# Kernel optimization log

Measured on AMD Instinct MI355X. Metric: run time of the kernel, lower is better.

## Reference

```python
import math
import jax, jax.numpy as jnp
import numpy as np

B, L, D, H = 2, 2048, 1024, 16
DK = D // H
N_TYPES = 6  # token types; < 3 => prompt (U/O/E), >= 3 => item (I)


def setup_inputs() -> dict:
    key = jax.random.key(0)
    ks = jax.random.split(key, 8)
    w_scale = 0.02
    return {
        "x": jax.random.normal(ks[0], (B, L, D), dtype=jnp.float32),
        "token_types": jax.random.randint(ks[1], (B, L), 0, N_TYPES, dtype=jnp.int32),
        "seq_lens": jax.random.randint(ks[2], (B,), L // 2, L + 1, dtype=jnp.int32),
        "W_q": jax.random.normal(ks[3], (D, D), dtype=jnp.float32) * w_scale,
        "W_k": jax.random.normal(ks[4], (D, D), dtype=jnp.float32) * w_scale,
        "W_v": jax.random.normal(ks[5], (D, D), dtype=jnp.float32) * w_scale,
        "W_u": jax.random.normal(ks[6], (D, D), dtype=jnp.float32) * w_scale,
        "W_o": jax.random.normal(ks[7], (D, D), dtype=jnp.float32) * w_scale,
    }


def reference(x, token_types, seq_lens, W_q, W_k, W_v, W_u, W_o):
    b, l, d = x.shape
    neg = jnp.finfo(x.dtype).min

    def proj(W):  # torch Linear (no bias): y = x @ W.T -> (b, H, l, dk)
        return jnp.einsum("bld,ed->ble", x, W).reshape(b, l, H, DK).transpose(0, 2, 1, 3)

    Q, K, V, U = proj(W_q), proj(W_k), proj(W_v), proj(W_u)

    scores = jnp.einsum("bhid,bhjd->bhij", Q, K) / math.sqrt(DK)  # (b,H,l,l)

    # Hybrid mask: causal (-inf above diagonal), but 0 wherever key j is a
    # prompt token (prompt<->prompt bidirectional, item->prompt allowed).
    is_prompt = token_types < 3                      # (b, l)
    causal = jnp.where(jnp.triu(jnp.ones((l, l), dtype=bool), k=1), neg, 0.0).astype(x.dtype)
    mask = jnp.where(is_prompt[:, None, :], jnp.asarray(0.0, x.dtype), causal[None, :, :])  # (b,l,l)
    scores = scores + mask[:, None, :, :]

    # Padding mask on key positions j >= seq_len
    pad = jnp.arange(l)[None, :] >= seq_lens[:, None]  # (b, l)
    scores = jnp.where(pad[:, None, None, :], neg, scores)

    attn = jax.nn.softmax(scores, axis=-1)
    out = jnp.einsum("bhij,bhjd->bhid", attn, V) * U   # HSTU pointwise gating
    out = out.transpose(0, 2, 1, 3).reshape(b, l, d)
    return jnp.einsum("bld,ed->ble", out, W_o)
```

## Files before the change

kernel.cpp:

```cpp
#include <hip/hip_runtime.h>


#define L_SEQ 2048

typedef __attribute__((ext_vector_type(8))) short bf16x8;
typedef __attribute__((ext_vector_type(8))) unsigned short u16x8;
typedef __attribute__((ext_vector_type(4))) float f32x4;
typedef __attribute__((ext_vector_type(16))) float f32x16;

#if __has_builtin(__builtin_amdgcn_exp2f)
#define EXP2F __builtin_amdgcn_exp2f
#else
#define EXP2F __builtin_exp2f
#endif

__device__ __forceinline__ unsigned short f2bf(float f) {
  union { float f; unsigned u; } c; c.f = f;
  unsigned r = c.u + 0x7FFFu + ((c.u >> 16) & 1u);
  return (unsigned short)(r >> 16);
}
__device__ __forceinline__ float bf2f(unsigned short h) {
  union { unsigned u; float f; } c; c.u = ((unsigned)h) << 16;
  return c.f;
}

__device__ __forceinline__ void async16(const void* g, void* l) {
  __builtin_amdgcn_global_load_lds((__attribute__((address_space(1))) void*)g,
                                   (__attribute__((address_space(3))) void*)l,
                                   16, 0, 0);
}

__device__ __forceinline__ unsigned cvtpk_bf16(float lo, float hi) {
  unsigned r; asm("v_cvt_pk_bf16_f32 %0, %1, %2" : "=v"(r) : "v"(lo), "v"(hi));
  return r;
}

__global__ __launch_bounds__(256) void cvt_all(
    const float* __restrict__ x,
    const float* __restrict__ wq, const float* __restrict__ wk,
    const float* __restrict__ wv, const float* __restrict__ wu,
    const float* __restrict__ wo,
    unsigned short* __restrict__ xb, unsigned short* __restrict__ wcat,
    const int* __restrict__ tt, const int* __restrict__ sl,
    unsigned* __restrict__ allowed) {
  if (blockIdx.x >= 9216) {
    const int k = blockIdx.x - 9216;
    const int wv64 = (k << 2) + (threadIdx.x >> 6);
    const int b = wv64 >> 5, w32 = wv64 & 31;
    const int lane = threadIdx.x & 63;
    const int j = w32 * 64 + lane;
    const unsigned long long m = __ballot((tt[b * L_SEQ + j] < 3) && (j < sl[b]));
    if (lane == 0) {
      allowed[b * 64 + 2 * w32]     = (unsigned)m;
      allowed[b * 64 + 2 * w32 + 1] = (unsigned)(m >> 32);
    }
    return;
  }
  const int seg = blockIdx.x >> 10;
  const float* s;
  unsigned short* d;
  float sc = 1.0f;
  if (seg < 4)      { s = x + (size_t)seg * 1048576;  d = xb + (size_t)seg * 1048576; }
  else {
    const int ws = seg - 4;
    s = ws == 0 ? wq : ws == 1 ? wk : ws == 2 ? wv : ws == 3 ? wu : wo;
    d = wcat + (size_t)ws * 1048576;
    if (ws == 0) sc = 0.18033688011112042f;
  }
  const int i = ((blockIdx.x & 1023) * 256 + threadIdx.x) * 4;
  const float4 v = *reinterpret_cast<const float4*>(s + i);
  ushort4 o;
  o.x = f2bf(v.x * sc); o.y = f2bf(v.y * sc); o.z = f2bf(v.z * sc); o.w = f2bf(v.w * sc);
  *reinterpret_cast<ushort4*>(d + i) = o;
}

__global__ __launch_bounds__(512, 2) void gemm256_bt(
    const unsigned short* __restrict__ A,
    const unsigned short* __restrict__ BT,
    unsigned short* __restrict__ Cb, int K)
{
  __shared__ char smem[131072];

  const int tid = threadIdx.x, w = tid >> 6, lane = tid & 63;
  const int lo = lane & 15, hi = lane >> 4;
  const int wm = w >> 2, wn = w & 3;
  const int d = blockIdx.x;
  const int lin = (d & 7) * 32 + (d >> 3);
  const int i0 = (lin >> 4) * 256, j0 = (lin & 15) * 256;

  const int rr = lane >> 3, ch = lane & 7;
  const int ksw = 8 * (ch ^ rr);

  auto stage = [&](int buf, int t) {
    const size_t k0 = (size_t)t * 64 + ksw;
    #pragma unroll
    for (int q = 0; q < 2; ++q) {
      const int p = 2 * w + q;
      const int row = 8 * p + rr;
      #pragma unroll
      for (int h = 0; h < 2; ++h) {
        async16(A  + (size_t)(i0 + h * 128 + row) * K + k0,
                smem + buf * 32768 + h * 16384 + p * 1024);
        async16(BT + (size_t)(j0 + h * 128 + row) * K + k0,
                smem + 65536 + buf * 32768 + h * 16384 + p * 1024);
      }
    }
  };

  f32x4 acc[8][4] = {};
  stage(0, 0);

  const int nt = K >> 6;
  for (int u = 0; u < nt; ++u) {
    const int buf = u & 1;
    if (u + 1 < nt) {
      stage(buf ^ 1, u + 1);
      asm volatile("s_waitcnt vmcnt(8)" ::: "memory");
    } else {
      asm volatile("s_waitcnt vmcnt(0)" ::: "memory");
    }
    __builtin_amdgcn_s_barrier();
    __builtin_amdgcn_sched_barrier(0);

    const char* Ah = smem + buf * 32768 + wm * 16384;
    const char* Bh = smem + 65536 + buf * 32768 + (wn >> 1) * 16384;
    const int brow0 = (wn & 1) * 64;

    bf16x8 bfr[4][2];
    #pragma unroll
    for (int n = 0; n < 4; ++n)
      #pragma unroll
      for (int ks = 0; ks < 2; ++ks)
        bfr[n][ks] = *reinterpret_cast<const bf16x8*>(
            Bh + (brow0 + n * 16 + lo) * 128 + 16 * ((ks * 4 + hi) ^ (lo & 7)));

    #pragma unroll
    for (int ph = 0; ph < 4; ++ph) {
      bf16x8 afr[2][2];
      #pragma unroll
      for (int mm = 0; mm < 2; ++mm)
        #pragma unroll
        for (int ks = 0; ks < 2; ++ks)
          afr[mm][ks] = *reinterpret_cast<const bf16x8*>(
              Ah + ((ph * 2 + mm) * 16 + lo) * 128 + 16 * ((ks * 4 + hi) ^ (lo & 7)));
      __builtin_amdgcn_s_barrier();
      __builtin_amdgcn_sched_barrier(0);
      __builtin_amdgcn_s_setprio(1);
      #pragma unroll
      for (int ks = 0; ks < 2; ++ks)
        #pragma unroll
        for (int mm = 0; mm < 2; ++mm)
          #pragma unroll
          for (int n = 0; n < 4; ++n)
            acc[ph * 2 + mm][n] = __builtin_amdgcn_mfma_f32_16x16x32_bf16(
                afr[mm][ks], bfr[n][ks], acc[ph * 2 + mm][n], 0, 0, 0);
      __builtin_amdgcn_s_setprio(0);
      __builtin_amdgcn_s_barrier();
      __builtin_amdgcn_sched_barrier(0);
    }
  }

  const int mi = (lin & 15) >> 2;
  const int cb0 = j0 & 1023;
  if (mi != 2) {
    unsigned short* base = Cb + (size_t)mi * 4194304;
    #pragma unroll
    for (int m = 0; m < 8; ++m) {
      const int row = i0 + wm * 128 + m * 16 + hi * 4;
      #pragma unroll
      for (int n = 0; n < 4; ++n) {
        const int col = cb0 + wn * 64 + n * 16 + lo;
        #pragma unroll
        for (int r = 0; r < 4; ++r)
          base[(size_t)(row + r) * 1024 + col] = f2bf(acc[m][n][r]);
      }
    }
  } else {
    #pragma unroll
    for (int m = 0; m < 8; ++m) {
      const int tl = (wm << 1) + (m >> 2);
      #pragma unroll
      for (int n = 0; n < 4; ++n) {
        const int dd = n * 16 + lo;
        char* ib = smem + (tl * 4 + wn) * 8192 + dd * 128;
        const int swd = dd & 7;
        #pragma unroll
        for (int r = 0; r < 4; ++r) {
          const int k = (m * 16 + hi * 4 + r) & 63;
          *(unsigned short*)(ib + 16 * ((k >> 3) ^ swd) + 2 * (k & 7)) =
              f2bf(acc[m][n][r]);
        }
      }
    }
    __builtin_amdgcn_s_barrier();
    unsigned short* V = Cb + (size_t)2 * 4194304;
    const int bI = i0 >> 11;
    const int t0 = (i0 & 2047) >> 6;
    const int h0 = cb0 >> 6;
    #pragma unroll
    for (int img = 0; img < 16; ++img) {
      const int tl = img >> 2, hl = img & 3;
      const size_t ob = ((size_t)(bI * 16 + h0 + hl) * 32 + (t0 + tl)) * 4096;
      *reinterpret_cast<u16x8*>(V + ob + tid * 8) =
          *reinterpret_cast<const u16x8*>(smem + img * 8192 + tid * 16);
    }
  }
}

template<int OUT_BF16, int MF>
__global__ __launch_bounds__(256) void gemm_bt(
    const unsigned short* __restrict__ A,
    const unsigned short* __restrict__ BT,
    float* __restrict__ Cf, unsigned short* __restrict__ Cb,
    int M, int N, int K, int cpx, int nbxm, int nbxs)
{
  __shared__ unsigned short As[2][MF * 32 * 32];
  __shared__ unsigned short Bs[2][128 * 32];

  const int tid = threadIdx.x;
  const int w = tid >> 6, lane = tid & 63;
  const int lo = lane & 15, hi = lane >> 4;
  const int d = blockIdx.x + gridDim.x * blockIdx.y;
  const int lin = (d & 7) * cpx + (d >> 3);
  const int i0 = (lin >> nbxs) * (MF * 32), j0 = (lin & nbxm) * 128;
  const int wr = w >> 1, wc = w & 1;
  const int rsub = lane >> 2, csub = (lane & 3) * 8;

  f32x4 acc[MF][4] = {};

  auto stage = [&](int buf, int k0) {
    #pragma unroll
    for (int q = 0; q < 2; ++q) {
      const int cB = w * 2 + q;
      async16(BT + (size_t)(j0 + cB * 16 + rsub) * K + k0 + csub, &Bs[buf][cB * 512]);
      if (q < MF / 2) {
        const int cA = w * (MF / 2) + q;
        async16(A + (size_t)(i0 + cA * 16 + rsub) * K + k0 + csub, &As[buf][cA * 512]);
      }
    }
  };

  stage(0, 0);
  __syncthreads();

  const int nt = K >> 5;
  for (int t = 0; t < nt; ++t) {
    const int buf = t & 1;
    if (t + 1 < nt) stage(buf ^ 1, (t + 1) << 5);
    bf16x8 a[MF], b[4];
    #pragma unroll
    for (int m = 0; m < MF; ++m)
      a[m] = *reinterpret_cast<const bf16x8*>(
          &As[buf][(wr * (MF * 16) + m * 16 + lo) * 32 + hi * 8]);
    #pragma unroll
    for (int n = 0; n < 4; ++n)
      b[n] = *reinterpret_cast<const bf16x8*>(&Bs[buf][(wc * 64 + n * 16 + lo) * 32 + hi * 8]);
    #pragma unroll
    for (int m = 0; m < MF; ++m)
      #pragma unroll
      for (int n = 0; n < 4; ++n)
        acc[m][n] = __builtin_amdgcn_mfma_f32_16x16x32_bf16(a[m], b[n], acc[m][n], 0, 0, 0);
    __syncthreads();
  }

  #pragma unroll
  for (int m = 0; m < MF; ++m) {
    const int row = i0 + wr * (MF * 16) + m * 16 + hi * 4;
    #pragma unroll
    for (int n = 0; n < 4; ++n) {
      const int col = j0 + wc * 64 + n * 16 + lo;
      #pragma unroll
      for (int r = 0; r < 4; ++r) {
        if (OUT_BF16) Cb[(size_t)(row + r) * N + col] = f2bf(acc[m][n][r]);
        else          Cf[(size_t)(row + r) * N + col] = acc[m][n][r];
      }
    }
  }
}

#define FINZ(SS, ZZ)                                                          \
  {                                                                           \
    if (fast) {                                                               \
      _Pragma("unroll")                                                       \
      for (int r = 0; r < 16; ++r) { SS[r] = EXP2F(SS[r]); rs += SS[r]; }     \
    } else {                                                                  \
      const unsigned pmz = __builtin_amdgcn_readlane(pmword, 2 * t + ZZ);     \
      const int lim = limb - j0 - 32 * ZZ;                                    \
      const unsigned cm = lim < 0 ? 0u : (lim >= 31 ? ~0u : ((2u << lim) - 1u)); \
      const unsigned al = (pmz >> (4 * sb)) | cm;                             \
      _Pragma("unroll")                                                       \
      for (int r = 0; r < 16; ++r) {                                          \
        const int kc = (r & 3) + 8 * (r >> 2);                                \
        const float p = EXP2F(SS[r]);                                         \
        SS[r] = ((al >> kc) & 1) ? p : 0.f;                                   \
        rs += SS[r];                                                          \
      }                                                                       \
    }                                                                         \
    unsigned U0, U1, W0, W1;                                                  \
    U0 = cvtpk_bf16(SS[0], SS[1]);  U1 = cvtpk_bf16(SS[2], SS[3]);            \
    W0 = cvtpk_bf16(SS[4], SS[5]);  W1 = cvtpk_bf16(SS[6], SS[7]);            \
    asm("v_permlane32_swap_b32 %0, %1" : "+v"(U0), "+v"(W0));                 \
    asm("v_permlane32_swap_b32 %0, %1" : "+v"(U1), "+v"(W1));                 \
    union { unsigned u[4]; bf16x8 v; } pu;                                    \
    pu.u[0] = U0; pu.u[1] = U1; pu.u[2] = W0; pu.u[3] = W1;                   \
    const bf16x8 pfA = pu.v;                                                  \
    U0 = cvtpk_bf16(SS[8], SS[9]);   U1 = cvtpk_bf16(SS[10], SS[11]);         \
    W0 = cvtpk_bf16(SS[12], SS[13]); W1 = cvtpk_bf16(SS[14], SS[15]);         \
    asm("v_permlane32_swap_b32 %0, %1" : "+v"(U0), "+v"(W0));                 \
    asm("v_permlane32_swap_b32 %0, %1" : "+v"(U1), "+v"(W1));                 \
    pu.u[0] = U0; pu.u[1] = U1; pu.u[2] = W0; pu.u[3] = W1;                   \
    const bf16x8 pfB = pu.v;                                                  \
    const int swA = ((4 * ZZ + sb) ^ (c & 7)) << 4;                           \
    const int swB = ((4 * ZZ + 2 + sb) ^ (c & 7)) << 4;                       \
    const bf16x8 va0 = *reinterpret_cast<const bf16x8*>(Vb + c * 128 + swA);  \
    const bf16x8 va1 = *reinterpret_cast<const bf16x8*>(Vb + (32 + c) * 128 + swA); \
    const bf16x8 vb0 = *reinterpret_cast<const bf16x8*>(Vb + c * 128 + swB);  \
    const bf16x8 vb1 = *reinterpret_cast<const bf16x8*>(Vb + (32 + c) * 128 + swB); \
    __builtin_amdgcn_s_setprio(1);                                            \
    o0 = __builtin_amdgcn_mfma_f32_32x32x16_bf16(va0, pfA, o0, 0, 0, 0);      \
    o1 = __builtin_amdgcn_mfma_f32_32x32x16_bf16(va1, pfA, o1, 0, 0, 0);      \
    o0 = __builtin_amdgcn_mfma_f32_32x32x16_bf16(vb0, pfB, o0, 0, 0, 0);      \
    o1 = __builtin_amdgcn_mfma_f32_32x32x16_bf16(vb1, pfB, o1, 0, 0, 0);      \
    __builtin_amdgcn_s_setprio(0);                                            \
  }

__global__ __launch_bounds__(512, 4) void hstu_attn(
    const unsigned short* __restrict__ qm,
    const unsigned short* __restrict__ km,
    const unsigned short* __restrict__ vimg,
    const unsigned short* __restrict__ um,
    const unsigned* __restrict__ allowed,
    const int* __restrict__ slens,
    unsigned short* __restrict__ gated)
{
  __shared__ char smem[65536];

  const int dlin = blockIdx.x + (blockIdx.y << 4) + (blockIdx.z << 8);
  const int lin = ((dlin & 7) << 6) | (dlin >> 3);
  const int qt = lin & 15, h = (lin >> 4) & 15, b = lin >> 8;
  const int i0 = qt * 128;
  const int tid = threadIdx.x, w = tid >> 6, lane = tid & 63;
  const int g = w >> 2, wq = w & 3;
  const int c = lane & 31, sb = lane >> 5;
  const int seqlen = slens[b];
  const size_t rbm = (size_t)b * L_SEQ * 1024;
  const size_t vbg = (size_t)(b * 16 + h) * 32 * 4096;
  const int qrow = i0 + wq * 32 + c;

  auto stageK = [&](int buf, int t) {
    const int j0 = t * 64;
    char* Kb = smem + (g * 2 + buf) * 8192;
    #pragma unroll
    for (int q = 0; q < 2; ++q) {
      const int p = wq * 2 + q;
      const int krow = 8 * p + (lane >> 3);
      const int d0 = 8 * ((lane & 7) ^ (lane >> 3));
      async16(km + rbm + (size_t)(j0 + krow) * 1024 + h * 64 + d0, Kb + p * 1024);
    }
  };
  auto stageV = [&](int buf, int t) {
    char* Vb = smem + 32768 + (g * 2 + buf) * 8192;
    #pragma unroll
    for (int q = 0; q < 2; ++q) {
      const int p = wq * 2 + q;
      async16(vimg + vbg + (size_t)t * 4096 + p * 512 + lane * 8, Vb + p * 1024);
    }
  };

  const int nt = (seqlen + 63) >> 6;
  const int niter = (nt + 1) >> 1;

  stageK(0, g); stageV(0, g);

  bf16x8 qf[4];
  #pragma unroll
  for (int kd = 0; kd < 4; ++kd)
    qf[kd] = *reinterpret_cast<const bf16x8*>(
        qm + rbm + (size_t)qrow * 1024 + h * 64 + kd * 16 + sb * 8);
  const unsigned pmword = allowed[b * 64 + lane];
  const int limb = (qrow < seqlen - 1 ? qrow : seqlen - 1) - 4 * sb;

  f32x16 o0 = {}, o1 = {};
  float rs = 0.f;

  asm volatile("s_waitcnt vmcnt(0)" ::: "memory");
  __builtin_amdgcn_s_barrier();
  __builtin_amdgcn_sched_barrier(0);

  for (int i = 0; i < niter; ++i) {
    const int t = 2 * i + g;
    const bool active = t < nt;
    const int buf = i & 1;
    const int j0 = t * 64;
    const bool pre = (t + 2 < nt);

    if (active) {
      if (pre) { stageK(buf ^ 1, t + 2); stageV(buf ^ 1, t + 2); }

      const char* Kb = smem + (g * 2 + buf) * 8192;
      const char* Vb = smem + 32768 + (g * 2 + buf) * 8192;
      const bool fast = (j0 + 64 <= seqlen) && (j0 + 63 <= i0 + wq * 32);

      f32x16 sE = {}, sO = {};
      __builtin_amdgcn_s_setprio(1);
      #pragma unroll
      for (int kd = 0; kd < 4; ++kd) {
        const int sw = ((2 * kd + sb) ^ (c & 7)) << 4;
        const bf16x8 kfE = *reinterpret_cast<const bf16x8*>(Kb + c * 128 + sw);
        const bf16x8 kfO = *reinterpret_cast<const bf16x8*>(Kb + (32 + c) * 128 + sw);
        sE = __builtin_amdgcn_mfma_f32_32x32x16_bf16(kfE, qf[kd], sE, 0, 0, 0);
        sO = __builtin_amdgcn_mfma_f32_32x32x16_bf16(kfO, qf[kd], sO, 0, 0, 0);
      }
      __builtin_amdgcn_s_setprio(0);

      FINZ(sE, 0)
      FINZ(sO, 1)

      asm volatile("s_waitcnt vmcnt(0)" ::: "memory");
    }
    __builtin_amdgcn_s_barrier();
    __builtin_amdgcn_sched_barrier(0);
  }

  const float lsum = rs + __shfl_xor(rs, 32, 64);

  float* cb = (float*)smem;
  const int col = wq * 64 + lane;
  if (g == 1) {
    #pragma unroll
    for (int r = 0; r < 16; ++r) {
      cb[r * 260 + col]        = o0[r];
      cb[(16 + r) * 260 + col] = o1[r];
    }
    cb[32 * 260 + col] = lsum;
  }
  __syncthreads();
  if (g == 1) return;
  #pragma unroll
  for (int r = 0; r < 16; ++r) {
    o0[r] += cb[r * 260 + col];
    o1[r] += cb[(16 + r) * 260 + col];
  }
  const float rin = 1.0f / (lsum + cb[32 * 260 + col]);

  #pragma unroll
  for (int n = 0; n < 2; ++n) {
    const f32x16 o = n ? o1 : o0;
    #pragma unroll
    for (int rq = 0; rq < 4; ++rq) {
      const int d0 = n * 32 + 8 * rq + 4 * sb;
      const ushort4 uu = *reinterpret_cast<const ushort4*>(
          um + rbm + (size_t)qrow * 1024 + h * 64 + d0);
      ushort4 gg;
      gg.x = f2bf(o[4 * rq + 0] * rin * bf2f(uu.x));
      gg.y = f2bf(o[4 * rq + 1] * rin * bf2f(uu.y));
      gg.z = f2bf(o[4 * rq + 2] * rin * bf2f(uu.z));
      gg.w = f2bf(o[4 * rq + 3] * rin * bf2f(uu.w));
      *reinterpret_cast<ushort4*>(
          gated + (size_t)(b * L_SEQ + qrow) * 1024 + h * 64 + d0) = gg;
    }
  }
}

extern "C" void kernel_launch(void* const* d_in, const int* in_sizes, int n_in,
                              void* d_out, int out_size, void* d_ws, size_t ws_size,
                              hipStream_t stream) {
  const float* x  = (const float*)d_in[0];
  const int* tt   = (const int*)d_in[1];
  const int* sl   = (const int*)d_in[2];
  const float* Wq = (const float*)d_in[3];
  const float* Wk = (const float*)d_in[4];
  const float* Wv = (const float*)d_in[5];
  const float* Wu = (const float*)d_in[6];
  const float* Wo = (const float*)d_in[7];
  float* out = (float*)d_out;

  unsigned* allowed     = (unsigned*)d_ws;
  unsigned short* xb    = (unsigned short*)d_ws + 256;
  unsigned short* wcat  = xb    + (size_t)4096 * 1024;
  unsigned short* wob   = wcat  + (size_t)4096 * 1024;
  unsigned short* qkvu  = wob   + (size_t)1024 * 1024;
  unsigned short* gated = qkvu  + (size_t)4096 * 4096;

  cvt_all<<<9232, 256, 0, stream>>>(x, Wq, Wk, Wv, Wu, Wo, xb, wcat,
                                    tt, sl, allowed);

  gemm256_bt<<<256, 512, 0, stream>>>(xb, wcat, qkvu, 1024);

  hstu_attn<<<dim3(16, 16, 2), 512, 0, stream>>>(
      qkvu, qkvu + (size_t)4194304, qkvu + (size_t)2 * 4194304,
      qkvu + (size_t)3 * 4194304, allowed, sl, gated);

  gemm_bt<0, 2><<<dim3(8, 64), 256, 0, stream>>>(gated, wob, out, nullptr,
                                                 4096, 1024, 1024, 64, 7, 3);
}
```

Baseline: 118.1 us.

## Triple-buffer K tiles so K prefetch runs two tiles ahead of V

Reworks the attention loop's shared-memory staging. K now uses a three-buffer ring and is prefetched two tiles ahead, while V stays double-buffered one tile ahead. The loop waits with vmcnt(2) so the newest K load can remain in flight across the barrier. This aims to hide global-load latency for K behind more compute, at the cost of more LDS per block (80KB vs 64KB), which may reduce occupancy.

```diff
diff --git a/kernel.cpp b/kernel.cpp
--- a/kernel.cpp
+++ b/kernel.cpp
@@ -314,13 +314,13 @@
     const int swB = ((4 * ZZ + 2 + sb) ^ (c & 7)) << 4;                       \
     const bf16x8 va0 = *reinterpret_cast<const bf16x8*>(Vb + c * 128 + swA);  \
     const bf16x8 va1 = *reinterpret_cast<const bf16x8*>(Vb + (32 + c) * 128 + swA); \
-    const bf16x8 vb0 = *reinterpret_cast<const bf16x8*>(Vb + c * 128 + swB);  \
-    const bf16x8 vb1 = *reinterpret_cast<const bf16x8*>(Vb + (32 + c) * 128 + swB); \
+    const bf16x8 vb0_ = *reinterpret_cast<const bf16x8*>(Vb + c * 128 + swB); \
+    const bf16x8 vb1_ = *reinterpret_cast<const bf16x8*>(Vb + (32 + c) * 128 + swB); \
     __builtin_amdgcn_s_setprio(1);                                            \
     o0 = __builtin_amdgcn_mfma_f32_32x32x16_bf16(va0, pfA, o0, 0, 0, 0);      \
     o1 = __builtin_amdgcn_mfma_f32_32x32x16_bf16(va1, pfA, o1, 0, 0, 0);      \
-    o0 = __builtin_amdgcn_mfma_f32_32x32x16_bf16(vb0, pfB, o0, 0, 0, 0);      \
-    o1 = __builtin_amdgcn_mfma_f32_32x32x16_bf16(vb1, pfB, o1, 0, 0, 0);      \
+    o0 = __builtin_amdgcn_mfma_f32_32x32x16_bf16(vb0_, pfB, o0, 0, 0, 0);     \
+    o1 = __builtin_amdgcn_mfma_f32_32x32x16_bf16(vb1_, pfB, o1, 0, 0, 0);     \
     __builtin_amdgcn_s_setprio(0);                                            \
   }
 
@@ -333,7 +333,7 @@
     const int* __restrict__ slens,
     unsigned short* __restrict__ gated)
 {
-  __shared__ char smem[65536];
+  __shared__ char smem[81920];
 
   const int dlin = blockIdx.x + (blockIdx.y << 4) + (blockIdx.z << 8);
   const int lin = ((dlin & 7) << 6) | (dlin >> 3);
@@ -347,9 +347,15 @@
   const size_t vbg = (size_t)(b * 16 + h) * 32 * 4096;
   const int qrow = i0 + wq * 32 + c;
 
-  auto stageK = [&](int buf, int t) {
+  char* const gb = smem + g * 40960;
+  char* kb0 = gb;
+  char* kb1 = gb + 8192;
+  char* kb2 = gb + 16384;
+  char* vb0 = gb + 24576;
+  char* vb1 = gb + 32768;
+
+  auto stageK = [&](char* Kb, int t) {
     const int j0 = t * 64;
-    char* Kb = smem + (g * 2 + buf) * 8192;
     #pragma unroll
     for (int q = 0; q < 2; ++q) {
       const int p = wq * 2 + q;
@@ -358,8 +364,7 @@
       async16(km + rbm + (size_t)(j0 + krow) * 1024 + h * 64 + d0, Kb + p * 1024);
     }
   };
-  auto stageV = [&](int buf, int t) {
-    char* Vb = smem + 32768 + (g * 2 + buf) * 8192;
+  auto stageV = [&](char* Vb, int t) {
     #pragma unroll
     for (int q = 0; q < 2; ++q) {
       const int p = wq * 2 + q;
@@ -369,8 +374,9 @@
 
   const int nt = (seqlen + 63) >> 6;
   const int niter = (nt + 1) >> 1;
-
-  stageK(0, g); stageV(0, g);
+  const int myn = (nt - g + 1) >> 1;
+
+  stageK(kb0, g); stageK(kb1, g + 2); stageV(vb0, g);
 
   bf16x8 qf[4];
   #pragma unroll
@@ -389,16 +395,15 @@
 
   for (int i = 0; i < niter; ++i) {
     const int t = 2 * i + g;
-    const bool active = t < nt;
-    const int buf = i & 1;
-    const int j0 = t * 64;
-    const bool pre = (t + 2 < nt);
+    const bool active = i < myn;
 
     if (active) {
-      if (pre) { stageK(buf ^ 1, t + 2); stageV(buf ^ 1, t + 2); }
-
-      const char* Kb = smem + (g * 2 + buf) * 8192;
-      const char* Vb = smem + 32768 + (g * 2 + buf) * 8192;
+      const int j0 = t * 64;
+      if (i + 1 < myn) stageV(vb1, t + 2);
+      if (i + 2 < myn) stageK(kb2, t + 4);
+
+      const char* Kb = kb0;
+      const char* Vb = vb0;
       const bool fast = (j0 + 64 <= seqlen) && (j0 + 63 <= i0 + wq * 32);
 
       f32x16 sE = {}, sO = {};
@@ -416,10 +421,13 @@
       FINZ(sE, 0)
       FINZ(sO, 1)
 
-      asm volatile("s_waitcnt vmcnt(0)" ::: "memory");
+      if (i + 2 < myn) { asm volatile("s_waitcnt vmcnt(2)" ::: "memory"); }
+      else             { asm volatile("s_waitcnt vmcnt(0)" ::: "memory"); }
     }
     __builtin_amdgcn_s_barrier();
     __builtin_amdgcn_sched_barrier(0);
+    char* tk = kb0; kb0 = kb1; kb1 = kb2; kb2 = tk;
+    char* tv = vb0; vb0 = vb1; vb1 = tv;
   }
 
   const float lsum = rs + __shfl_xor(rs, 32, 64);
```

Result: no change. 119.0 us (+0.8%).
